# Optimization experiments

Measured on AMD Instinct MI355X. Metric: run time of the kernel, lower is better.

## Reference

```python
import jax, jax.numpy as jnp
import numpy as np

D, HS, HE, E, K = 1024, 2048, 1024, 8, 2   # d_model, shared hidden (d_ff//2), expert hidden (d_ff//4), n_experts, top_k
B, T = 4, 1024
N_SHARED = 1


def setup_inputs() -> dict:
    key = jax.random.key(0)
    ks = jax.random.split(key, 9)
    g = lambda k, shape, s: jax.random.normal(k, shape, jnp.float32) * s
    return {
        "x": g(ks[0], (B, T, D), 1.0),
        "t_emb": g(ks[1], (B, D), 1.0),
        "router_W": g(ks[2], (2 * D, E), 0.01),      # torch Linear(2C->E, bias=False), std=0.01 init
        "router_bias": jnp.zeros((E,), jnp.float32),  # load-balance bias buffer
        "w1": g(ks[3], (D, HS), 0.02),                # shared expert SwiGLU
        "w3": g(ks[4], (D, HS), 0.02),
        "w2": g(ks[5], (HS, D), 0.02),
        "W1e": g(ks[6], (E, D, HE), 0.02),            # routed experts, Linear->GELU->Linear
        "W2e": g(ks[7], (E, HE, D), 0.02),
    }


def reference(x, t_emb, router_W, router_bias, w1, w3, w2, W1e, W2e):
    Bb, Tt, C = x.shape
    xf = x.reshape(-1, C)                                              # [N, C]
    tf = jnp.broadcast_to(t_emb[:, None, :], (Bb, Tt, C)).reshape(-1, C)
    N = xf.shape[0]

    shared = (jax.nn.silu(xf @ w1) * (xf @ w3)) @ w2                   # [N, C]

    # router affinity (sigmoid, fp32)
    s = jax.nn.sigmoid((jnp.concatenate([xf, tf], axis=-1) @ router_W).astype(jnp.float32))
    sel_scores = s + router_bias                                       # [N, E]
    _, topk_idx = jax.lax.top_k(sel_scores, K)                         # [N, K]

    # gates normalized over selected raw affinities
    s_sel = jnp.take_along_axis(s, topk_idx, axis=1)                   # [N, K]
    denom = s_sel.sum(axis=1, keepdims=True)
    gates = jnp.where(denom > 1e-9, s_sel / (denom + 1e-9), 1.0 / K).astype(x.dtype)

    # combine weights [N, E]: scatter gates to selected experts
    combine = jnp.zeros((N, E), x.dtype).at[jnp.arange(N)[:, None], topk_idx].add(gates)

    # dense expert evaluation (reference form of grouped GEMM + scatter-combine)
    h = jax.nn.gelu(jnp.einsum('nc,ech->enh', xf, W1e), approximate=False)  # [E, N, He]
    y = jnp.einsum('enh,ehc->enc', h, W2e)                                   # [E, N, C]
    routed = jnp.einsum('ne,enc->nc', combine, y)                            # [N, C]

    return ((shared + routed) / (N_SHARED + K)).reshape(Bb, Tt, C)
```

## Files before the change

### kernel.cpp

```cpp
#include <hip/hip_runtime.h>
#include <hip/hip_bf16.h>
#include <math.h>

#define D_MODEL 1024
#define HS 2048
#define HE 1024
#define NEXP 8
#define NTOK 4096
#define NSLOT 8192

typedef __attribute__((ext_vector_type(4))) float f32x4;
typedef __attribute__((ext_vector_type(8))) short bf16x8;

__device__ __forceinline__ short f2b(float f) {
  __hip_bfloat16 h = __float2bfloat16(f);
  return *reinterpret_cast<short*>(&h);
}
__device__ __forceinline__ float b2f(short s) {
  return __bfloat162float(*reinterpret_cast<__hip_bfloat16*>(&s));
}

__device__ __forceinline__ void gl_lds16(const short* g, short* l) {
  __builtin_amdgcn_global_load_lds(
      (const __attribute__((address_space(1))) void*)g,
      (__attribute__((address_space(3))) void*)l, 16, 0, 0);
}

__device__ __forceinline__ void tr_tile(const float* __restrict__ in,
                                        short* __restrict__ out, int R, int C,
                                        int bx, int by, int bz, int rmap,
                                        float (*tile)[69], int t) {
  const int c0 = bx * 64;
  const int r0 = by * 64;
  const size_t bo = (size_t)bz * R * C;
  const int lr = t >> 4;
  const int lc4 = (t & 15) * 4;
#pragma unroll
  for (int i = 0; i < 4; i++) {
    const float4 v = *(const float4*)&in[bo + (size_t)(r0 + lr + i * 16) * C + c0 + lc4];
    tile[lc4 + 0][lr + i * 16] = v.x;
    tile[lc4 + 1][lr + i * 16] = v.y;
    tile[lc4 + 2][lr + i * 16] = v.z;
    tile[lc4 + 3][lr + i * 16] = v.w;
  }
  __syncthreads();
#pragma unroll
  for (int i = 0; i < 4; i++) {
    const int oc = (t >> 4) + i * 16;
    const int or4 = (t & 15) * 4;
    short4 o;
    o.x = f2b(tile[oc][or4 + 0]);
    o.y = f2b(tile[oc][or4 + 1]);
    o.z = f2b(tile[oc][or4 + 2]);
    o.w = f2b(tile[oc][or4 + 3]);
    const int c = c0 + oc;
    size_t orow;
    if (rmap == 0) orow = bo + (size_t)c * R;
    else orow = (size_t)((c >> 5) * 64 + (rmap == 2 ? 32 : 0) + (c & 31)) * R;
    *(short4*)&out[orow + r0 + or4] = o;
  }
}

__global__ __launch_bounds__(256) void tr_all(
    const float* __restrict__ w1, const float* __restrict__ w3,
    const float* __restrict__ w2, const float* __restrict__ W1e,
    const float* __restrict__ W2e, short* __restrict__ w13I,
    short* __restrict__ w2T, short* __restrict__ W1eT, short* __restrict__ W2eT) {
  __shared__ float tile[64][69];
  const int id = blockIdx.x;
  const int t = threadIdx.x;
  if (id < 1024) {
    const int z = id >> 9, rem = id & 511;
    tr_tile(z ? w3 : w1, w13I, D_MODEL, HS, rem & 31, rem >> 5, 0, z ? 2 : 1, tile, t);
  } else if (id < 1536) {
    const int rem = id - 1024;
    tr_tile(w2, w2T, HS, D_MODEL, rem & 15, rem >> 4, 0, 0, tile, t);
  } else {
    const int rem = id - 1536;
    const int z = rem >> 8, r2 = rem & 255;
    if (z < 8)
      tr_tile(W1e, W1eT, D_MODEL, HE, r2 & 15, r2 >> 4, z, 0, tile, t);
    else
      tr_tile(W2e, W2eT, HE, D_MODEL, r2 & 15, r2 >> 4, z - 8, 0, tile, t);
  }
}

__global__ __launch_bounds__(256) void router_kernel(
    const float* __restrict__ x, const float* __restrict__ temb,
    const float* __restrict__ rw, const float* __restrict__ rbias,
    short* __restrict__ xb, int* __restrict__ topk, float* __restrict__ gates) {
  const int t = (blockIdx.x * 256 + threadIdx.x) >> 6;
  const int lane = threadIdx.x & 63;
  const float* xr = x + (size_t)t * D_MODEL;
  const float* tr = temb + (size_t)(t >> 10) * D_MODEL;
  float acc[NEXP] = {};
#pragma unroll
  for (int i = 0; i < 4; i++) {
    const int j = i * 256 + lane * 4;
    const float4 xv = *(const float4*)&xr[j];
    const float4 tv = *(const float4*)&tr[j];
    short4 o;
    o.x = f2b(xv.x); o.y = f2b(xv.y); o.z = f2b(xv.z); o.w = f2b(xv.w);
    *(short4*)&xb[(size_t)t * D_MODEL + j] = o;
    const float* wx = rw + (size_t)j * NEXP;
    const float* wt = rw + (size_t)(D_MODEL + j) * NEXP;
    const float xa[4] = {xv.x, xv.y, xv.z, xv.w};
    const float ta[4] = {tv.x, tv.y, tv.z, tv.w};
#pragma unroll
    for (int u = 0; u < 4; u++)
#pragma unroll
      for (int e = 0; e < NEXP; e++)
        acc[e] += xa[u] * wx[u * NEXP + e] + ta[u] * wt[u * NEXP + e];
  }
#pragma unroll
  for (int off = 32; off; off >>= 1)
#pragma unroll
    for (int e = 0; e < NEXP; e++) acc[e] += __shfl_xor(acc[e], off);
  if (lane == 0) {
    float s[NEXP], sel[NEXP];
#pragma unroll
    for (int e = 0; e < NEXP; e++) {
      s[e] = 1.f / (1.f + expf(-acc[e]));
      sel[e] = s[e] + rbias[e];
    }
    int i0 = 0;
#pragma unroll
    for (int e = 1; e < NEXP; e++) if (sel[e] > sel[i0]) i0 = e;
    int i1 = (i0 == 0) ? 1 : 0;
#pragma unroll
    for (int e = 0; e < NEXP; e++) if (e != i0 && sel[e] > sel[i1]) i1 = e;
    float s0 = s[i0], s1 = s[i1], den = s0 + s1;
    float g0, g1;
    if (den > 1e-9f) { g0 = s0 / (den + 1e-9f); g1 = s1 / (den + 1e-9f); }
    else { g0 = 0.5f; g1 = 0.5f; }
    topk[t * 2] = i0; topk[t * 2 + 1] = i1;
    gates[t * 2] = g0; gates[t * 2 + 1] = g1;
  }
}

__global__ __launch_bounds__(1024) void group_kernel(const int* __restrict__ topk,
                                                     int* __restrict__ perm,
                                                     int* __restrict__ offs,
                                                     int* __restrict__ te,
                                                     int* __restrict__ tm,
                                                     int* __restrict__ ntile) {
  __shared__ int cnt[NEXP], cur[NEXP];
  const int t = threadIdx.x;
  if (t < NEXP) cnt[t] = 0;
  __syncthreads();
  int mye[8];
#pragma unroll
  for (int i = 0; i < 8; i++) {
    mye[i] = topk[i * 1024 + t];
    atomicAdd(&cnt[mye[i]], 1);
  }
  __syncthreads();
  if (t == 0) {
    int a = 0;
    for (int e = 0; e < NEXP; e++) { offs[e] = a; cur[e] = a; a += cnt[e]; }
    offs[NEXP] = a;
    int nt = 0;
    for (int e = 0; e < NEXP; e++)
      for (int m0 = 0; m0 < cnt[e]; m0 += 128) { te[nt] = e; tm[nt] = m0; nt++; }
    ntile[0] = nt;
  }
  __syncthreads();
#pragma unroll
  for (int i = 0; i < 8; i++) {
    int pos = atomicAdd(&cur[mye[i]], 1);
    perm[pos] = i * 1024 + t;
  }
}

__global__ __launch_bounds__(256, 4) void moe_k1(
    const short* __restrict__ xb, const short* __restrict__ w13I,
    const short* __restrict__ W1eT, short* __restrict__ ubuf,
    short* __restrict__ hexpb, const int* __restrict__ perm,
    const int* __restrict__ offs, const int* __restrict__ te,
    const int* __restrict__ tm, const int* __restrict__ ntile) {
  extern __shared__ short lds[];
  const int td = threadIdx.x;
  const int id = blockIdx.x;
  const bool isG1 = id < 1024;
  int m_panel = 0, n_panel = 0, m0 = 0, rbeg = 0, rend = 0, bxn = 0;
  const short* A;
  const short* Bb;
  if (isG1) {
    const int xcd = id & 7, w = id >> 3;
    n_panel = xcd * 4 + (w >> 5);
    m_panel = w & 31;
    A = xb;
    Bb = w13I + (size_t)n_panel * 128 * 1024;
  } else {
    const int g = id - 1024;
    const int ty = g >> 3;
    if (ty >= ntile[0]) return;
    bxn = g & 7;
    const int e = te[ty];
    m0 = tm[ty];
    rbeg = offs[e]; rend = offs[e + 1];
    A = xb;
    Bb = W1eT + ((size_t)e * 1024 + bxn * 128) * 1024;
  }

  const int srow = td >> 2;
  const int colsw = ((td & 3) ^ ((td >> 4) & 3)) * 8;
  const short* a0p;
  const short* a1p;
  {
    int g0, g1;
    if (isG1) { g0 = m_panel * 128 + srow; g1 = g0 + 64; }
    else {
      g0 = perm[min(rbeg + m0 + srow, rend - 1)] >> 1;
      g1 = perm[min(rbeg + m0 + 64 + srow, rend - 1)] >> 1;
    }
    a0p = A + (size_t)g0 * 1024 + colsw;
    a1p = A + (size_t)g1 * 1024 + colsw;
  }
  const short* b0p = Bb + (size_t)srow * 1024 + colsw;
  const short* b1p = Bb + (size_t)(64 + srow) * 1024 + colsw;

#define K1STAGE(t_, b_)                                             \
  do {                                                              \
    gl_lds16(a0p + (t_) * 32, lds + (b_) * 8192 + td * 8);          \
    gl_lds16(a1p + (t_) * 32, lds + (b_) * 8192 + 2048 + td * 8);   \
    gl_lds16(b0p + (t_) * 32, lds + (b_) * 8192 + 4096 + td * 8);   \
    gl_lds16(b1p + (t_) * 32, lds + (b_) * 8192 + 6144 + td * 8);   \
  } while (0)

  const int l = td & 63;
  const int wv = td >> 6;
  const int wm = (wv >> 1) * 64, wn = (wv & 1) * 64;
  const int lr = l & 15;
  const int kg = l >> 4;

#define SWO(r_) ((unsigned)((r_) * 32 + ((kg ^ (((r_) >> 2) & 3)) * 8)))
#define LDA1(mf_) (*(const bf16x8*)&Ah[SWO(wm + (mf_)*16 + lr)])
#define LDB1(nf_) (*(const bf16x8*)&Bh[SWO(wn + (nf_)*16 + lr)])
#define MM1(mf_, a_)                                                                   \
  acc[mf_][0] = __builtin_amdgcn_mfma_f32_16x16x32_bf16(a_, b0, acc[mf_][0], 0, 0, 0); \
  acc[mf_][1] = __builtin_amdgcn_mfma_f32_16x16x32_bf16(a_, b1, acc[mf_][1], 0, 0, 0); \
  acc[mf_][2] = __builtin_amdgcn_mfma_f32_16x16x32_bf16(a_, b2, acc[mf_][2], 0, 0, 0); \
  acc[mf_][3] = __builtin_amdgcn_mfma_f32_16x16x32_bf16(a_, b3, acc[mf_][3], 0, 0, 0)

  f32x4 acc[4][4] = {};

  K1STAGE(0, 0);
  for (int t = 0; t < 32; ++t) {
    const int p = t & 1, q = p ^ 1;
    const short* Ah = lds + p * 8192;
    const short* Bh = lds + p * 8192 + 4096;
    if (t < 31) {
      K1STAGE(t + 1, q);
      asm volatile("s_waitcnt vmcnt(4)" ::: "memory");
    } else {
      asm volatile("s_waitcnt vmcnt(0)" ::: "memory");
    }
    __builtin_amdgcn_s_barrier();
    {
      bf16x8 b0 = LDB1(0), b1 = LDB1(1), b2 = LDB1(2), b3 = LDB1(3);
      bf16x8 a0 = LDA1(0), a1 = LDA1(1), a2 = LDA1(2), a3 = LDA1(3);
      __builtin_amdgcn_s_setprio(1);
      MM1(0, a0); MM1(1, a1); MM1(2, a2); MM1(3, a3);
      __builtin_amdgcn_s_setprio(0);
    }
    __builtin_amdgcn_sched_barrier(0);
    __builtin_amdgcn_s_barrier();
  }

  const int rq = (l >> 4) * 4;
  if (isG1) {
#pragma unroll
    for (int mf = 0; mf < 4; mf++)
#pragma unroll
      for (int j = 0; j < 4; j++) {
        const int row = m_panel * 128 + wm + mf * 16 + rq + j;
        short* Up = ubuf + (size_t)row * HS + n_panel * 64 + (wn >> 1) + lr;
#pragma unroll
        for (int nf = 0; nf < 2; nf++) {
          const float a = acc[mf][nf][j];
          const float b = acc[mf][nf + 2][j];
          Up[nf * 16] = f2b(a / (1.f + expf(-a)) * b);
        }
      }
  } else {
#pragma unroll
    for (int mf = 0; mf < 4; mf++)
#pragma unroll
      for (int j = 0; j < 4; j++) {
        const int gi = rbeg + m0 + wm + mf * 16 + rq + j;
        if (gi < rend) {
          short* Cp = hexpb + (size_t)gi * HE + bxn * 128 + wn + lr;
#pragma unroll
          for (int nf = 0; nf < 4; nf++) {
            const float v = acc[mf][nf][j];
            Cp[nf * 16] = f2b(0.5f * v * (1.0f + erff(v * 0.70710678118654752f)));
          }
        }
      }
  }
#undef K1STAGE
#undef SWO
#undef LDA1
#undef LDB1
#undef MM1
}

__global__ __launch_bounds__(256, 2) void moe_k2(
    const short* __restrict__ ubuf, const short* __restrict__ w2T,
    const short* __restrict__ hexpb, const short* __restrict__ W2eT,
    float* __restrict__ out, short* __restrict__ yb,
    const int* __restrict__ perm, const int* __restrict__ offs,
    const float* __restrict__ gates, const int* __restrict__ te,
    const int* __restrict__ tm, const int* __restrict__ ntile) {
  extern __shared__ short lds[];
  const int td = threadIdx.x;
  const int id = blockIdx.x;
  const bool isG2 = id < 256;
  int m_panel = 0, n_panel = 0, m0 = 0, rbeg = 0, rend = 0, bxn = 0, NT, K;
  const short* A;
  const short* Bb;
  if (isG2) {
    const int xcd = id & 7, slot = id >> 3;
    n_panel = slot & 7;
    m_panel = xcd * 4 + (slot >> 3);
    A = ubuf;
    K = HS; NT = 32;
    Bb = w2T + (size_t)n_panel * 128 * HS;
  } else {
    const int g = id - 256;
    const int ty = g >> 3;
    if (ty >= ntile[0]) return;
    bxn = g & 7;
    const int e = te[ty];
    m0 = tm[ty];
    rbeg = offs[e]; rend = offs[e + 1];
    A = hexpb;
    K = HE; NT = 16;
    Bb = W2eT + ((size_t)e * 1024 + bxn * 128) * 1024;
  }

  const int srow = td >> 3;
  const int colsw8 = ((td & 7) ^ (srow & 7)) * 8;
  const short* ap[4];
  const short* bp[4];
#pragma unroll
  for (int u = 0; u < 4; u++) {
    const int trow = u * 32 + srow;
    int grow;
    if (isG2) grow = m_panel * 128 + trow;
    else grow = min(rbeg + m0 + trow, rend - 1);
    ap[u] = A + (size_t)grow * K + colsw8;
    bp[u] = Bb + (size_t)trow * K + colsw8;
  }

#define K2STAGE(t_, b_)                                                    \
  do {                                                                     \
    gl_lds16(ap[0] + (t_) * 64, lds + (b_) * 16384 + td * 8);              \
    gl_lds16(ap[1] + (t_) * 64, lds + (b_) * 16384 + 2048 + td * 8);       \
    gl_lds16(ap[2] + (t_) * 64, lds + (b_) * 16384 + 4096 + td * 8);       \
    gl_lds16(ap[3] + (t_) * 64, lds + (b_) * 16384 + 6144 + td * 8);       \
    gl_lds16(bp[0] + (t_) * 64, lds + (b_) * 16384 + 8192 + td * 8);       \
    gl_lds16(bp[1] + (t_) * 64, lds + (b_) * 16384 + 10240 + td * 8);      \
    gl_lds16(bp[2] + (t_) * 64, lds + (b_) * 16384 + 12288 + td * 8);      \
    gl_lds16(bp[3] + (t_) * 64, lds + (b_) * 16384 + 14336 + td * 8);      \
  } while (0)

  const int l = td & 63;
  const int wv = td >> 6;
  const int wm = (wv >> 1) * 64, wn = (wv & 1) * 64;
  const int lr = l & 15;
  const int swzk0 = ((0 + (l >> 4) * 16) ^ ((l & 7) << 4)) >> 1;
  const int swzk1 = ((64 + (l >> 4) * 16) ^ ((l & 7) << 4)) >> 1;

#define LDA2(mf_, swz_) (*(const bf16x8*)&Ah[(unsigned)(((mf_)*16 + lr) * 64) + (swz_)])
#define LDB2(nf_, swz_) (*(const bf16x8*)&Bh[(unsigned)(((nf_)*16 + lr) * 64) + (swz_)])
#define MM2(mf_, a_)                                                                   \
  acc[mf_][0] = __builtin_amdgcn_mfma_f32_16x16x32_bf16(a_, b0, acc[mf_][0], 0, 0, 0); \
  acc[mf_][1] = __builtin_amdgcn_mfma_f32_16x16x32_bf16(a_, b1, acc[mf_][1], 0, 0, 0); \
  acc[mf_][2] = __builtin_amdgcn_mfma_f32_16x16x32_bf16(a_, b2, acc[mf_][2], 0, 0, 0); \
  acc[mf_][3] = __builtin_amdgcn_mfma_f32_16x16x32_bf16(a_, b3, acc[mf_][3], 0, 0, 0)

  f32x4 acc[4][4] = {};

  K2STAGE(0, 0);
  for (int t = 0; t < NT; ++t) {
    const int p = t & 1, q = p ^ 1;
    const short* Ah = lds + p * 16384 + wm * 64;
    const short* Bh = lds + p * 16384 + 8192 + wn * 64;
    if (t < NT - 1) {
      K2STAGE(t + 1, q);
      asm volatile("s_waitcnt vmcnt(8)" ::: "memory");
    } else {
      asm volatile("s_waitcnt vmcnt(0)" ::: "memory");
    }
    __builtin_amdgcn_s_barrier();
    {
      bf16x8 b0, b1, b2, b3, a0, a1, a2, a3;
      b0 = LDB2(0, swzk0); b1 = LDB2(1, swzk0); b2 = LDB2(2, swzk0); b3 = LDB2(3, swzk0);
      a0 = LDA2(0, swzk0); a1 = LDA2(1, swzk0); a2 = LDA2(2, swzk0); a3 = LDA2(3, swzk0);
      __builtin_amdgcn_s_setprio(1);
      MM2(0, a0); MM2(1, a1); MM2(2, a2); MM2(3, a3);
      __builtin_amdgcn_s_setprio(0);
      b0 = LDB2(0, swzk1); b1 = LDB2(1, swzk1); b2 = LDB2(2, swzk1); b3 = LDB2(3, swzk1);
      a0 = LDA2(0, swzk1); a1 = LDA2(1, swzk1); a2 = LDA2(2, swzk1); a3 = LDA2(3, swzk1);
      __builtin_amdgcn_s_setprio(1);
      MM2(0, a0); MM2(1, a1); MM2(2, a2); MM2(3, a3);
      __builtin_amdgcn_s_setprio(0);
    }
    __builtin_amdgcn_sched_barrier(0);
    __builtin_amdgcn_s_barrier();
  }

  const int rq = (l >> 4) * 4;
  if (isG2) {
#pragma unroll
    for (int mf = 0; mf < 4; mf++)
#pragma unroll
      for (int j = 0; j < 4; j++) {
        const int tok = m_panel * 128 + wm + mf * 16 + rq + j;
        float* Op = out + (size_t)tok * D_MODEL + n_panel * 128 + wn + lr;
#pragma unroll
        for (int nf = 0; nf < 4; nf++) Op[nf * 16] = acc[mf][nf][j];
      }
  } else {
#pragma unroll
    for (int mf = 0; mf < 4; mf++)
#pragma unroll
      for (int j = 0; j < 4; j++) {
        const int gi = rbeg + m0 + wm + mf * 16 + rq + j;
        if (gi < rend) {
          const int slot = perm[gi];
          const float g = gates[slot];
          short* Cp = yb + (size_t)slot * D_MODEL + bxn * 128 + wn + lr;
#pragma unroll
          for (int nf = 0; nf < 4; nf++) Cp[nf * 16] = f2b(g * acc[mf][nf][j]);
        }
      }
  }
#undef K2STAGE
#undef LDA2
#undef LDB2
#undef MM2
}

__global__ __launch_bounds__(256) void combine_kernel(float* __restrict__ out,
                                                      const short* __restrict__ yb) {
  const float inv3 = 1.0f / 3.0f;
#pragma unroll
  for (int rep = 0; rep < 2; rep++) {
    const int i = (rep * 2048 + blockIdx.x) * 256 + threadIdx.x;
    const int base = i * 4;
    const int tok = base >> 10;
    const int col = base & (D_MODEL - 1);
    float4 s = *(float4*)&out[base];
    const short4 y0 = *(const short4*)&yb[(size_t)(tok * 2) * D_MODEL + col];
    const short4 y1 = *(const short4*)&yb[(size_t)(tok * 2 + 1) * D_MODEL + col];
    s.x = (s.x + b2f(y0.x) + b2f(y1.x)) * inv3;
    s.y = (s.y + b2f(y0.y) + b2f(y1.y)) * inv3;
    s.z = (s.z + b2f(y0.z) + b2f(y1.z)) * inv3;
    s.w = (s.w + b2f(y0.w) + b2f(y1.w)) * inv3;
    *(float4*)&out[base] = s;
  }
}

extern "C" void kernel_launch(void* const* d_in, const int* in_sizes, int n_in,
                              void* d_out, int out_size, void* d_ws, size_t ws_size,
                              hipStream_t stream) {
  const float* x = (const float*)d_in[0];
  const float* temb = (const float*)d_in[1];
  const float* rw = (const float*)d_in[2];
  const float* rbias = (const float*)d_in[3];
  const float* w1 = (const float*)d_in[4];
  const float* w3 = (const float*)d_in[5];
  const float* w2 = (const float*)d_in[6];
  const float* W1e = (const float*)d_in[7];
  const float* W2e = (const float*)d_in[8];
  float* out = (float*)d_out;

  const size_t MB = 1ull << 20;
  char* w = (char*)d_ws;
  short* xb    = (short*)(w + 0 * MB);
  short* w13I  = (short*)(w + 8 * MB);
  short* w2T   = (short*)(w + 16 * MB);
  short* W1eT  = (short*)(w + 20 * MB);
  short* W2eT  = (short*)(w + 36 * MB);
  short* ubuf  = (short*)(w + 52 * MB);
  short* hexpb = (short*)(w + 68 * MB);
  short* yb    = (short*)(w + 84 * MB);
  float* gates = (float*)(w + 100 * MB);
  int* topk    = (int*)(w + 100 * MB + 32 * 1024);
  int* perm    = (int*)(w + 100 * MB + 64 * 1024);
  int* meta    = (int*)(w + 100 * MB + 96 * 1024);
  int* offs    = meta;
  int* te      = meta + 16;
  int* tm      = meta + 128;
  int* ntile   = meta + 256;

  hipFuncSetAttribute((const void*)&moe_k1,
                      hipFuncAttributeMaxDynamicSharedMemorySize, 32768);
  hipFuncSetAttribute((const void*)&moe_k2,
                      hipFuncAttributeMaxDynamicSharedMemorySize, 65536);

  tr_all<<<5632, 256, 0, stream>>>(w1, w3, w2, W1e, W2e, w13I, w2T, W1eT, W2eT);
  router_kernel<<<NTOK / 4, 256, 0, stream>>>(x, temb, rw, rbias, xb, topk, gates);
  group_kernel<<<1, 1024, 0, stream>>>(topk, perm, offs, te, tm, ntile);

  moe_k1<<<1600, 256, 32768, stream>>>(xb, w13I, W1eT, ubuf, hexpb, perm, offs,
                                       te, tm, ntile);

  moe_k2<<<832, 256, 65536, stream>>>(ubuf, w2T, hexpb, W2eT, out, yb, perm,
                                      offs, gates, te, tm, ntile);

  combine_kernel<<<2048, 256, 0, stream>>>(out, yb);
}
```

Measured before the change: 210.8 us.

## Widen GEMM tiles to 128x256 in moe_k1 and routed moe_k2 path

Doubles the N dimension of the block tile from 128 to 256 in moe_k1 (shared w1/w3 and routed first-layer GEMMs) and in the routed-expert branch of moe_k2. Each wave now computes 64x128 with a 4x8 accumulator array, so A tiles (especially gathered token rows) are loaded half as often and MFMA-to-LDS-load ratio rises. The shared SwiGLU epilogue index math is adjusted for the new interleaved column layout, and grid sizes drop accordingly. The cost is more registers and LDS per block (occupancy bound lowered from 4 to 2) and fewer blocks to fill the GPU.

```diff
diff --git a/kernel.cpp b/kernel.cpp
--- a/kernel.cpp
+++ b/kernel.cpp
@@ -172,7 +172,7 @@
   }
 }
 
-__global__ __launch_bounds__(256, 4) void moe_k1(
+__global__ __launch_bounds__(256, 2) void moe_k1(
     const short* __restrict__ xb, const short* __restrict__ w13I,
     const short* __restrict__ W1eT, short* __restrict__ ubuf,
     short* __restrict__ hexpb, const int* __restrict__ perm,
@@ -181,106 +181,111 @@
   extern __shared__ short lds[];
   const int td = threadIdx.x;
   const int id = blockIdx.x;
-  const bool isG1 = id < 1024;
+  const bool isG1 = id < 512;
   int m_panel = 0, n_panel = 0, m0 = 0, rbeg = 0, rend = 0, bxn = 0;
-  const short* A;
   const short* Bb;
   if (isG1) {
-    const int xcd = id & 7, w = id >> 3;
-    n_panel = xcd * 4 + (w >> 5);
+    const int x = id & 7, w = id >> 3;
+    n_panel = x * 2 + (w >> 5);
     m_panel = w & 31;
-    A = xb;
-    Bb = w13I + (size_t)n_panel * 128 * 1024;
+    Bb = w13I + (size_t)n_panel * 256 * 1024;
   } else {
-    const int g = id - 1024;
-    const int ty = g >> 3;
+    const int g = id - 512;
+    const int ty = g >> 2;
     if (ty >= ntile[0]) return;
-    bxn = g & 7;
+    bxn = g & 3;
     const int e = te[ty];
     m0 = tm[ty];
     rbeg = offs[e]; rend = offs[e + 1];
-    A = xb;
-    Bb = W1eT + ((size_t)e * 1024 + bxn * 128) * 1024;
+    Bb = W1eT + ((size_t)e * 1024 + bxn * 256) * 1024;
   }
 
   const int srow = td >> 2;
-  const int colsw = ((td & 3) ^ ((td >> 4) & 3)) * 8;
-  const short* a0p;
-  const short* a1p;
-  {
-    int g0, g1;
-    if (isG1) { g0 = m_panel * 128 + srow; g1 = g0 + 64; }
-    else {
-      g0 = perm[min(rbeg + m0 + srow, rend - 1)] >> 1;
-      g1 = perm[min(rbeg + m0 + 64 + srow, rend - 1)] >> 1;
-    }
-    a0p = A + (size_t)g0 * 1024 + colsw;
-    a1p = A + (size_t)g1 * 1024 + colsw;
-  }
-  const short* b0p = Bb + (size_t)srow * 1024 + colsw;
-  const short* b1p = Bb + (size_t)(64 + srow) * 1024 + colsw;
-
-#define K1STAGE(t_, b_)                                             \
-  do {                                                              \
-    gl_lds16(a0p + (t_) * 32, lds + (b_) * 8192 + td * 8);          \
-    gl_lds16(a1p + (t_) * 32, lds + (b_) * 8192 + 2048 + td * 8);   \
-    gl_lds16(b0p + (t_) * 32, lds + (b_) * 8192 + 4096 + td * 8);   \
-    gl_lds16(b1p + (t_) * 32, lds + (b_) * 8192 + 6144 + td * 8);   \
+  const int scol = ((td & 3) ^ ((srow >> 1) & 3)) * 8;
+  const short* ap[2];
+  const short* bp[4];
+#pragma unroll
+  for (int i = 0; i < 2; i++) {
+    const int row = i * 64 + srow;
+    int grow;
+    if (isG1) grow = m_panel * 128 + row;
+    else grow = perm[min(rbeg + m0 + row, rend - 1)] >> 1;
+    ap[i] = xb + (size_t)grow * 1024 + scol;
+  }
+#pragma unroll
+  for (int u = 0; u < 4; u++) bp[u] = Bb + (size_t)(u * 64 + srow) * 1024 + scol;
+
+#define K1STAGE(t_, b_)                                                \
+  do {                                                                 \
+    gl_lds16(ap[0] + (t_) * 32, lds + (b_) * 12288 + td * 8);          \
+    gl_lds16(ap[1] + (t_) * 32, lds + (b_) * 12288 + 2048 + td * 8);   \
+    gl_lds16(bp[0] + (t_) * 32, lds + (b_) * 12288 + 4096 + td * 8);   \
+    gl_lds16(bp[1] + (t_) * 32, lds + (b_) * 12288 + 6144 + td * 8);   \
+    gl_lds16(bp[2] + (t_) * 32, lds + (b_) * 12288 + 8192 + td * 8);   \
+    gl_lds16(bp[3] + (t_) * 32, lds + (b_) * 12288 + 10240 + td * 8);  \
   } while (0)
 
   const int l = td & 63;
   const int wv = td >> 6;
-  const int wm = (wv >> 1) * 64, wn = (wv & 1) * 64;
+  const int wm = wv >> 1;
+  const int wn = wv & 1;
   const int lr = l & 15;
   const int kg = l >> 4;
-
-#define SWO(r_) ((unsigned)((r_) * 32 + ((kg ^ (((r_) >> 2) & 3)) * 8)))
-#define LDA1(mf_) (*(const bf16x8*)&Ah[SWO(wm + (mf_)*16 + lr)])
-#define LDB1(nf_) (*(const bf16x8*)&Bh[SWO(wn + (nf_)*16 + lr)])
-#define MM1(mf_, a_)                                                                   \
-  acc[mf_][0] = __builtin_amdgcn_mfma_f32_16x16x32_bf16(a_, b0, acc[mf_][0], 0, 0, 0); \
-  acc[mf_][1] = __builtin_amdgcn_mfma_f32_16x16x32_bf16(a_, b1, acc[mf_][1], 0, 0, 0); \
-  acc[mf_][2] = __builtin_amdgcn_mfma_f32_16x16x32_bf16(a_, b2, acc[mf_][2], 0, 0, 0); \
-  acc[mf_][3] = __builtin_amdgcn_mfma_f32_16x16x32_bf16(a_, b3, acc[mf_][3], 0, 0, 0)
-
-  f32x4 acc[4][4] = {};
+  const int gsw = (kg ^ ((lr >> 1) & 3)) * 8;
+
+#define LDA1(mf_) (*(const bf16x8*)&Ah[(unsigned)((wm * 64 + (mf_)*16 + lr) * 32) + gsw])
+#define LDB1(nf_) (*(const bf16x8*)&Bh[(unsigned)((wn * 128 + (nf_)*16 + lr) * 32) + gsw])
+
+  f32x4 acc[4][8] = {};
 
   K1STAGE(0, 0);
+  asm volatile("s_waitcnt vmcnt(0)" ::: "memory");
+  __builtin_amdgcn_s_barrier();
+
   for (int t = 0; t < 32; ++t) {
     const int p = t & 1, q = p ^ 1;
-    const short* Ah = lds + p * 8192;
-    const short* Bh = lds + p * 8192 + 4096;
+    const short* Ah = lds + p * 12288;
+    const short* Bh = lds + p * 12288 + 4096;
     if (t < 31) {
       K1STAGE(t + 1, q);
-      asm volatile("s_waitcnt vmcnt(4)" ::: "memory");
+      asm volatile("s_waitcnt vmcnt(6)" ::: "memory");
     } else {
       asm volatile("s_waitcnt vmcnt(0)" ::: "memory");
     }
     __builtin_amdgcn_s_barrier();
     {
-      bf16x8 b0 = LDB1(0), b1 = LDB1(1), b2 = LDB1(2), b3 = LDB1(3);
-      bf16x8 a0 = LDA1(0), a1 = LDA1(1), a2 = LDA1(2), a3 = LDA1(3);
+      bf16x8 bf[8], af[4];
+#pragma unroll
+      for (int nf = 0; nf < 8; nf++) bf[nf] = LDB1(nf);
+#pragma unroll
+      for (int mf = 0; mf < 4; mf++) af[mf] = LDA1(mf);
       __builtin_amdgcn_s_setprio(1);
-      MM1(0, a0); MM1(1, a1); MM1(2, a2); MM1(3, a3);
+#pragma unroll
+      for (int mf = 0; mf < 4; mf++)
+#pragma unroll
+        for (int nf = 0; nf < 8; nf++)
+          acc[mf][nf] = __builtin_amdgcn_mfma_f32_16x16x32_bf16(af[mf], bf[nf],
+                                                                acc[mf][nf], 0, 0, 0);
       __builtin_amdgcn_s_setprio(0);
     }
     __builtin_amdgcn_sched_barrier(0);
     __builtin_amdgcn_s_barrier();
   }
 
-  const int rq = (l >> 4) * 4;
+  const int rq = kg * 4;
   if (isG1) {
 #pragma unroll
     for (int mf = 0; mf < 4; mf++)
 #pragma unroll
       for (int j = 0; j < 4; j++) {
-        const int row = m_panel * 128 + wm + mf * 16 + rq + j;
-        short* Up = ubuf + (size_t)row * HS + n_panel * 64 + (wn >> 1) + lr;
-#pragma unroll
-        for (int nf = 0; nf < 2; nf++) {
+        const int row = m_panel * 128 + wm * 64 + mf * 16 + rq + j;
+        short* Up = ubuf + (size_t)row * HS + n_panel * 128 + wn * 64;
+#pragma unroll
+        for (int pi = 0; pi < 4; pi++) {
+          const int nf = (pi & 1) + (pi >> 1) * 4;
           const float a = acc[mf][nf][j];
           const float b = acc[mf][nf + 2][j];
-          Up[nf * 16] = f2b(a / (1.f + expf(-a)) * b);
+          Up[(nf >> 2) * 32 + (nf & 1) * 16 + lr] = f2b(a / (1.f + expf(-a)) * b);
         }
       }
   } else {
@@ -288,11 +293,11 @@
     for (int mf = 0; mf < 4; mf++)
 #pragma unroll
       for (int j = 0; j < 4; j++) {
-        const int gi = rbeg + m0 + wm + mf * 16 + rq + j;
+        const int gi = rbeg + m0 + wm * 64 + mf * 16 + rq + j;
         if (gi < rend) {
-          short* Cp = hexpb + (size_t)gi * HE + bxn * 128 + wn + lr;
-#pragma unroll
-          for (int nf = 0; nf < 4; nf++) {
+          short* Cp = hexpb + (size_t)gi * HE + bxn * 256 + wn * 128 + lr;
+#pragma unroll
+          for (int nf = 0; nf < 8; nf++) {
             const float v = acc[mf][nf][j];
             Cp[nf * 16] = f2b(0.5f * v * (1.0f + erff(v * 0.70710678118654752f)));
           }
@@ -300,10 +305,8 @@
       }
   }
 #undef K1STAGE
-#undef SWO
 #undef LDA1
 #undef LDB1
-#undef MM1
 }
 
 __global__ __launch_bounds__(256, 2) void moe_k2(
@@ -316,44 +319,27 @@
   extern __shared__ short lds[];
   const int td = threadIdx.x;
   const int id = blockIdx.x;
-  const bool isG2 = id < 256;
-  int m_panel = 0, n_panel = 0, m0 = 0, rbeg = 0, rend = 0, bxn = 0, NT, K;
-  const short* A;
-  const short* Bb;
-  if (isG2) {
+  const int l = td & 63;
+  const int wv = td >> 6;
+  const int lr = l & 15;
+
+  if (id < 256) {
     const int xcd = id & 7, slot = id >> 3;
-    n_panel = slot & 7;
-    m_panel = xcd * 4 + (slot >> 3);
-    A = ubuf;
-    K = HS; NT = 32;
-    Bb = w2T + (size_t)n_panel * 128 * HS;
-  } else {
-    const int g = id - 256;
-    const int ty = g >> 3;
-    if (ty >= ntile[0]) return;
-    bxn = g & 7;
-    const int e = te[ty];
-    m0 = tm[ty];
-    rbeg = offs[e]; rend = offs[e + 1];
-    A = hexpb;
-    K = HE; NT = 16;
-    Bb = W2eT + ((size_t)e * 1024 + bxn * 128) * 1024;
-  }
-
-  const int srow = td >> 3;
-  const int colsw8 = ((td & 7) ^ (srow & 7)) * 8;
-  const short* ap[4];
-  const short* bp[4];
-#pragma unroll
-  for (int u = 0; u < 4; u++) {
-    const int trow = u * 32 + srow;
-    int grow;
-    if (isG2) grow = m_panel * 128 + trow;
-    else grow = min(rbeg + m0 + trow, rend - 1);
-    ap[u] = A + (size_t)grow * K + colsw8;
-    bp[u] = Bb + (size_t)trow * K + colsw8;
-  }
-
+    const int n_panel = slot & 7;
+    const int m_panel = xcd * 4 + (slot >> 3);
+    const short* A = ubuf;
+    const short* Bb = w2T + (size_t)n_panel * 128 * HS;
+
+    const int srow = td >> 3;
+    const int colsw8 = ((td & 7) ^ (srow & 7)) * 8;
+    const short* ap[4];
+    const short* bp[4];
+#pragma unroll
+    for (int u = 0; u < 4; u++) {
+      const int trow = u * 32 + srow;
+      ap[u] = A + (size_t)(m_panel * 128 + trow) * HS + colsw8;
+      bp[u] = Bb + (size_t)trow * HS + colsw8;
+    }
 #define K2STAGE(t_, b_)                                                    \
   do {                                                                     \
     gl_lds16(ap[0] + (t_) * 64, lds + (b_) * 16384 + td * 8);              \
@@ -365,14 +351,9 @@
     gl_lds16(bp[2] + (t_) * 64, lds + (b_) * 16384 + 12288 + td * 8);      \
     gl_lds16(bp[3] + (t_) * 64, lds + (b_) * 16384 + 14336 + td * 8);      \
   } while (0)
-
-  const int l = td & 63;
-  const int wv = td >> 6;
-  const int wm = (wv >> 1) * 64, wn = (wv & 1) * 64;
-  const int lr = l & 15;
-  const int swzk0 = ((0 + (l >> 4) * 16) ^ ((l & 7) << 4)) >> 1;
-  const int swzk1 = ((64 + (l >> 4) * 16) ^ ((l & 7) << 4)) >> 1;
-
+    const int wm = (wv >> 1) * 64, wn = (wv & 1) * 64;
+    const int swzk0 = ((0 + (l >> 4) * 16) ^ ((l & 7) << 4)) >> 1;
+    const int swzk1 = ((64 + (l >> 4) * 16) ^ ((l & 7) << 4)) >> 1;
 #define LDA2(mf_, swz_) (*(const bf16x8*)&Ah[(unsigned)(((mf_)*16 + lr) * 64) + (swz_)])
 #define LDB2(nf_, swz_) (*(const bf16x8*)&Bh[(unsigned)(((nf_)*16 + lr) * 64) + (swz_)])
 #define MM2(mf_, a_)                                                                   \
@@ -380,40 +361,36 @@
   acc[mf_][1] = __builtin_amdgcn_mfma_f32_16x16x32_bf16(a_, b1, acc[mf_][1], 0, 0, 0); \
   acc[mf_][2] = __builtin_amdgcn_mfma_f32_16x16x32_bf16(a_, b2, acc[mf_][2], 0, 0, 0); \
   acc[mf_][3] = __builtin_amdgcn_mfma_f32_16x16x32_bf16(a_, b3, acc[mf_][3], 0, 0, 0)
-
-  f32x4 acc[4][4] = {};
-
-  K2STAGE(0, 0);
-  for (int t = 0; t < NT; ++t) {
-    const int p = t & 1, q = p ^ 1;
-    const short* Ah = lds + p * 16384 + wm * 64;
-    const short* Bh = lds + p * 16384 + 8192 + wn * 64;
-    if (t < NT - 1) {
-      K2STAGE(t + 1, q);
-      asm volatile("s_waitcnt vmcnt(8)" ::: "memory");
-    } else {
-      asm volatile("s_waitcnt vmcnt(0)" ::: "memory");
-    }
-    __builtin_amdgcn_s_barrier();
-    {
-      bf16x8 b0, b1, b2, b3, a0, a1, a2, a3;
-      b0 = LDB2(0, swzk0); b1 = LDB2(1, swzk0); b2 = LDB2(2, swzk0); b3 = LDB2(3, swzk0);
-      a0 = LDA2(0, swzk0); a1 = LDA2(1, swzk0); a2 = LDA2(2, swzk0); a3 = LDA2(3, swzk0);
-      __builtin_amdgcn_s_setprio(1);
-      MM2(0, a0); MM2(1, a1); MM2(2, a2); MM2(3, a3);
-      __builtin_amdgcn_s_setprio(0);
-      b0 = LDB2(0, swzk1); b1 = LDB2(1, swzk1); b2 = LDB2(2, swzk1); b3 = LDB2(3, swzk1);
-      a0 = LDA2(0, swzk1); a1 = LDA2(1, swzk1); a2 = LDA2(2, swzk1); a3 = LDA2(3, swzk1);
-      __builtin_amdgcn_s_setprio(1);
-      MM2(0, a0); MM2(1, a1); MM2(2, a2); MM2(3, a3);
-      __builtin_amdgcn_s_setprio(0);
-    }
-    __builtin_amdgcn_sched_barrier(0);
-    __builtin_amdgcn_s_barrier();
-  }
-
-  const int rq = (l >> 4) * 4;
-  if (isG2) {
+    f32x4 acc[4][4] = {};
+    K2STAGE(0, 0);
+    for (int t = 0; t < 32; ++t) {
+      const int p = t & 1, q = p ^ 1;
+      const short* Ah = lds + p * 16384 + wm * 64;
+      const short* Bh = lds + p * 16384 + 8192 + wn * 64;
+      if (t < 31) {
+        K2STAGE(t + 1, q);
+        asm volatile("s_waitcnt vmcnt(8)" ::: "memory");
+      } else {
+        asm volatile("s_waitcnt vmcnt(0)" ::: "memory");
+      }
+      __builtin_amdgcn_s_barrier();
+      {
+        bf16x8 b0, b1, b2, b3, a0, a1, a2, a3;
+        b0 = LDB2(0, swzk0); b1 = LDB2(1, swzk0); b2 = LDB2(2, swzk0); b3 = LDB2(3, swzk0);
+        a0 = LDA2(0, swzk0); a1 = LDA2(1, swzk0); a2 = LDA2(2, swzk0); a3 = LDA2(3, swzk0);
+        __builtin_amdgcn_s_setprio(1);
+        MM2(0, a0); MM2(1, a1); MM2(2, a2); MM2(3, a3);
+        __builtin_amdgcn_s_setprio(0);
+        b0 = LDB2(0, swzk1); b1 = LDB2(1, swzk1); b2 = LDB2(2, swzk1); b3 = LDB2(3, swzk1);
+        a0 = LDA2(0, swzk1); a1 = LDA2(1, swzk1); a2 = LDA2(2, swzk1); a3 = LDA2(3, swzk1);
+        __builtin_amdgcn_s_setprio(1);
+        MM2(0, a0); MM2(1, a1); MM2(2, a2); MM2(3, a3);
+        __builtin_amdgcn_s_setprio(0);
+      }
+      __builtin_amdgcn_sched_barrier(0);
+      __builtin_amdgcn_s_barrier();
+    }
+    const int rq = (l >> 4) * 4;
 #pragma unroll
     for (int mf = 0; mf < 4; mf++)
 #pragma unroll
@@ -423,25 +400,98 @@
 #pragma unroll
         for (int nf = 0; nf < 4; nf++) Op[nf * 16] = acc[mf][nf][j];
       }
-  } else {
-#pragma unroll
-    for (int mf = 0; mf < 4; mf++)
-#pragma unroll
-      for (int j = 0; j < 4; j++) {
-        const int gi = rbeg + m0 + wm + mf * 16 + rq + j;
-        if (gi < rend) {
-          const int slot = perm[gi];
-          const float g = gates[slot];
-          short* Cp = yb + (size_t)slot * D_MODEL + bxn * 128 + wn + lr;
-#pragma unroll
-          for (int nf = 0; nf < 4; nf++) Cp[nf * 16] = f2b(g * acc[mf][nf][j]);
-        }
-      }
-  }
 #undef K2STAGE
 #undef LDA2
 #undef LDB2
 #undef MM2
+  } else {
+    const int g = id - 256;
+    const int ty = g >> 2;
+    if (ty >= ntile[0]) return;
+    const int bxn = g & 3;
+    const int e = te[ty];
+    const int m0 = tm[ty];
+    const int rbeg = offs[e], rend = offs[e + 1];
+    const short* Bb = W2eT + ((size_t)e * 1024 + bxn * 256) * 1024;
+
+    const int srow = td >> 2;
+    const int scol = ((td & 3) ^ ((srow >> 1) & 3)) * 8;
+    const short* ap[2];
+    const short* bp[4];
+#pragma unroll
+    for (int i = 0; i < 2; i++) {
+      const int grow = min(rbeg + m0 + i * 64 + srow, rend - 1);
+      ap[i] = hexpb + (size_t)grow * 1024 + scol;
+    }
+#pragma unroll
+    for (int u = 0; u < 4; u++) bp[u] = Bb + (size_t)(u * 64 + srow) * 1024 + scol;
+
+#define G2STAGE(t_, b_)                                                \
+  do {                                                                 \
+    gl_lds16(ap[0] + (t_) * 32, lds + (b_) * 12288 + td * 8);          \
+    gl_lds16(ap[1] + (t_) * 32, lds + (b_) * 12288 + 2048 + td * 8);   \
+    gl_lds16(bp[0] + (t_) * 32, lds + (b_) * 12288 + 4096 + td * 8);   \
+    gl_lds16(bp[1] + (t_) * 32, lds + (b_) * 12288 + 6144 + td * 8);   \
+    gl_lds16(bp[2] + (t_) * 32, lds + (b_) * 12288 + 8192 + td * 8);   \
+    gl_lds16(bp[3] + (t_) * 32, lds + (b_) * 12288 + 10240 + td * 8);  \
+  } while (0)
+    const int wm = wv >> 1;
+    const int wn = wv & 1;
+    const int kg = l >> 4;
+    const int gsw = (kg ^ ((lr >> 1) & 3)) * 8;
+#define LDA3(mf_) (*(const bf16x8*)&Ah[(unsigned)((wm * 64 + (mf_)*16 + lr) * 32) + gsw])
+#define LDB3(nf_) (*(const bf16x8*)&Bh[(unsigned)((wn * 128 + (nf_)*16 + lr) * 32) + gsw])
+    f32x4 acc[4][8] = {};
+    G2STAGE(0, 0);
+    asm volatile("s_waitcnt vmcnt(0)" ::: "memory");
+    __builtin_amdgcn_s_barrier();
+    for (int t = 0; t < 32; ++t) {
+      const int p = t & 1, q = p ^ 1;
+      const short* Ah = lds + p * 12288;
+      const short* Bh = lds + p * 12288 + 4096;
+      if (t < 31) {
+        G2STAGE(t + 1, q);
+        asm volatile("s_waitcnt vmcnt(6)" ::: "memory");
+      } else {
+        asm volatile("s_waitcnt vmcnt(0)" ::: "memory");
+      }
+      __builtin_amdgcn_s_barrier();
+      {
+        bf16x8 bf[8], af[4];
+#pragma unroll
+        for (int nf = 0; nf < 8; nf++) bf[nf] = LDB3(nf);
+#pragma unroll
+        for (int mf = 0; mf < 4; mf++) af[mf] = LDA3(mf);
+        __builtin_amdgcn_s_setprio(1);
+#pragma unroll
+        for (int mf = 0; mf < 4; mf++)
+#pragma unroll
+          for (int nf = 0; nf < 8; nf++)
+            acc[mf][nf] = __builtin_amdgcn_mfma_f32_16x16x32_bf16(af[mf], bf[nf],
+                                                                  acc[mf][nf], 0, 0, 0);
+        __builtin_amdgcn_s_setprio(0);
+      }
+      __builtin_amdgcn_sched_barrier(0);
+      __builtin_amdgcn_s_barrier();
+    }
+    const int rq = kg * 4;
+#pragma unroll
+    for (int mf = 0; mf < 4; mf++)
+#pragma unroll
+      for (int j = 0; j < 4; j++) {
+        const int gi = rbeg + m0 + wm * 64 + mf * 16 + rq + j;
+        if (gi < rend) {
+          const int slot = perm[gi];
+          const float gt = gates[slot];
+          short* Cp = yb + (size_t)slot * D_MODEL + bxn * 256 + wn * 128 + lr;
+#pragma unroll
+          for (int nf = 0; nf < 8; nf++) Cp[nf * 16] = f2b(gt * acc[mf][nf][j]);
+        }
+      }
+#undef G2STAGE
+#undef LDA3
+#undef LDB3
+  }
 }
 
 __global__ __launch_bounds__(256) void combine_kernel(float* __restrict__ out,
@@ -498,7 +548,7 @@
   int* ntile   = meta + 256;
 
   hipFuncSetAttribute((const void*)&moe_k1,
-                      hipFuncAttributeMaxDynamicSharedMemorySize, 32768);
+                      hipFuncAttributeMaxDynamicSharedMemorySize, 49152);
   hipFuncSetAttribute((const void*)&moe_k2,
                       hipFuncAttributeMaxDynamicSharedMemorySize, 65536);
 
@@ -506,10 +556,10 @@
   router_kernel<<<NTOK / 4, 256, 0, stream>>>(x, temb, rw, rbias, xb, topk, gates);
   group_kernel<<<1, 1024, 0, stream>>>(topk, perm, offs, te, tm, ntile);
 
-  moe_k1<<<1600, 256, 32768, stream>>>(xb, w13I, W1eT, ubuf, hexpb, perm, offs,
-                                       te, tm, ntile);
-
-  moe_k2<<<832, 256, 65536, stream>>>(ubuf, w2T, hexpb, W2eT, out, yb, perm,
+  moe_k1<<<800, 256, 49152, stream>>>(xb, w13I, W1eT, ubuf, hexpb, perm, offs,
+                                      te, tm, ntile);
+
+  moe_k2<<<544, 256, 65536, stream>>>(ubuf, w2T, hexpb, W2eT, out, yb, perm,
                                       offs, gates, te, tm, ntile);
 
   combine_kernel<<<2048, 256, 0, stream>>>(out, yb);
```

After: 216.9 us. 2.9% more time.
